# Optimization experiments

Hardware: AMD Instinct MI355X
Metric: run time of the kernel (lower is better)

The kernel has to match this reference:

```python
import jax, jax.numpy as jnp
import numpy as np

N, E, G = 10000, 160000, 64
NODE_DIM, HID = 128, 256


def _edge_conv(x, src, dst, w1, b1, w2, b2):
    # gather endpoints: x_i = target features, x_j = source features (PyG source_to_target)
    x_i = x[dst]                              # [E, C]
    x_j = x[src]                              # [E, C]
    m = jnp.concatenate([x_i, x_j - x_i], axis=-1)  # [E, 2C]
    m = jax.nn.relu(m @ w1 + b1) @ w2 + b2          # [E, H]
    out = jax.ops.segment_max(m, dst, num_segments=N)  # scatter-max per target node
    return out  # nodes with no in-edges get -inf; subsequent relu maps them to 0 (matches PyG fill 0 + relu)


def setup_inputs() -> dict:
    key = jax.random.key(0)
    ks = jax.random.split(key, 20)
    x = jax.random.normal(ks[0], (N, NODE_DIM), dtype=jnp.float32)
    edge_index = jax.random.randint(ks[1], (2, E), 0, N)
    batch = jnp.sort(jax.random.randint(ks[2], (N,), 0, G))
    s = 0.05
    inp = {"x": x, "edge_index": edge_index, "batch": batch}
    dims = [(2 * NODE_DIM, HID), (2 * HID, HID), (2 * HID, HID)]
    for li, (din, dout) in enumerate(dims):
        inp[f"c{li}_w1"] = jax.random.normal(ks[3 + 4 * li], (din, dout), jnp.float32) * s
        inp[f"c{li}_b1"] = jnp.zeros((dout,), jnp.float32)
        inp[f"c{li}_w2"] = jax.random.normal(ks[4 + 4 * li], (dout, dout), jnp.float32) * s
        inp[f"c{li}_b2"] = jnp.zeros((dout,), jnp.float32)
    inp["cl_w1"] = jax.random.normal(ks[15], (2 * HID, HID), jnp.float32) * s
    inp["cl_b1"] = jnp.zeros((HID,), jnp.float32)
    inp["cl_w2"] = jax.random.normal(ks[16], (HID, 64), jnp.float32) * s
    inp["cl_b2"] = jnp.zeros((64,), jnp.float32)
    inp["cl_w3"] = jax.random.normal(ks[17], (64, 1), jnp.float32) * s
    inp["cl_b3"] = jnp.zeros((1,), jnp.float32)
    return inp


def reference(x, edge_index, batch,
              c0_w1, c0_b1, c0_w2, c0_b2,
              c1_w1, c1_b1, c1_w2, c1_b2,
              c2_w1, c2_b1, c2_w2, c2_b2,
              cl_w1, cl_b1, cl_w2, cl_b2, cl_w3, cl_b3):
    src, dst = edge_index[0], edge_index[1]
    for (w1, b1, w2, b2) in [(c0_w1, c0_b1, c0_w2, c0_b2),
                             (c1_w1, c1_b1, c1_w2, c1_b2),
                             (c2_w1, c2_b1, c2_w2, c2_b2)]:
        x = jax.nn.relu(_edge_conv(x, src, dst, w1, b1, w2, b2))
    # global mean / max pool per graph
    sums = jax.ops.segment_sum(x, batch, num_segments=G)
    counts = jax.ops.segment_sum(jnp.ones((x.shape[0], 1), x.dtype), batch, num_segments=G)
    x_mean = sums / jnp.maximum(counts, 1.0)
    x_max = jax.ops.segment_max(x, batch, num_segments=G)
    x_max = jnp.where(counts > 0, x_max, 0.0)
    h = jnp.concatenate([x_mean, x_max], axis=1)  # [G, 2H]
    h = jax.nn.relu(h @ cl_w1 + cl_b1)            # dropout is eval-mode identity
    h = jax.nn.relu(h @ cl_w2 + cl_b2)
    out = (h @ cl_w3 + cl_b3).squeeze(-1)         # [G]
    return out
```

## Files before the change

### kernel.cpp

```cpp
#include <hip/hip_runtime.h>


#define NN 10000
#define NE 160000
#define NG 64
#define NP 10048
#define EB 64

typedef __attribute__((ext_vector_type(8))) _Float16 f16x8;
typedef __attribute__((ext_vector_type(4))) _Float16 f16x4;
typedef __attribute__((ext_vector_type(4))) float f32x4;

__global__ void hist_kernel(const int* __restrict__ dstI, int* __restrict__ hist) {
    int i = blockIdx.x * blockDim.x + threadIdx.x;
    if (i < NE) atomicAdd(&hist[dstI[i]], 1);
}

__global__ void scan_kernel(const int* __restrict__ hist, int* __restrict__ cursor) {
    __shared__ int sums[256];
    const int t = threadIdx.x;
    const int per = (NN + 255) / 256;
    const int lo = t * per, hi = (lo + per < NN) ? lo + per : NN;
    int s = 0;
    for (int i = lo; i < hi; ++i) s += hist[i];
    sums[t] = s;
    __syncthreads();
    for (int ofs = 1; ofs < 256; ofs <<= 1) {
        int add = (t >= ofs) ? sums[t - ofs] : 0;
        __syncthreads();
        sums[t] += add;
        __syncthreads();
    }
    int run = sums[t] - s;
    for (int i = lo; i < hi; ++i) {
        int h = hist[i];
        cursor[i] = run;
        run += h;
    }
}

__global__ void scatter_kernel(const int* __restrict__ srcI, const int* __restrict__ dstI,
                               int* __restrict__ cursor,
                               int* __restrict__ se2, int* __restrict__ de2) {
    int i = blockIdx.x * blockDim.x + threadIdx.x;
    if (i < NE) {
        int d = dstI[i];
        int p = atomicAdd(&cursor[d], 1);
        se2[p] = srcI[i];
        de2[p] = d;
    }
}

__global__ void prep_weights(const float* __restrict__ w1, const float* __restrict__ w2, int C,
                             _Float16* __restrict__ WcT, _Float16* __restrict__ w2T) {
    int total1 = 512 * C;
    int total = total1 + 256 * 256;
    for (int i = blockIdx.x * blockDim.x + threadIdx.x; i < total; i += gridDim.x * blockDim.x) {
        if (i < total1) {
            int n = i / C, k = i - n * C;
            float v = (n < 256) ? (w1[k * 256 + n] - w1[(C + k) * 256 + n])
                                : w1[(C + k) * 256 + (n - 256)];
            WcT[n * C + k] = (_Float16)v;
        } else {
            int j = i - total1;
            int n = j >> 8, k = j & 255;
            w2T[n * 256 + k] = (_Float16)w2[k * 256 + n];
        }
    }
}

template <int C>
__global__ __launch_bounds__(256) void node_gemm(
    const float* __restrict__ xf, const _Float16* __restrict__ WT,
    const float* __restrict__ b1, float* __restrict__ Af, _Float16* __restrict__ Bh) {
    const int wave = threadIdx.x >> 6, lane = threadIdx.x & 63;
    const int lrow = lane & 15, lk = (lane >> 4) * 8;
    const int r0 = blockIdx.x * 64;
    const int c0 = blockIdx.y * 256 + wave * 64;

    f32x4 acc[4][4] = {};
#pragma unroll
    for (int kk = 0; kk < C; kk += 32) {
        f16x8 ah[4];
#pragma unroll
        for (int m = 0; m < 4; ++m) {
            int rc = r0 + m * 16 + lrow;
            if (rc > NN - 1) rc = NN - 1;
            const float* xp = xf + (size_t)rc * C + kk + lk;
            const float4 v0 = *(const float4*)(xp);
            const float4 v1 = *(const float4*)(xp + 4);
            f16x8 a;
            a[0] = (_Float16)v0.x; a[1] = (_Float16)v0.y;
            a[2] = (_Float16)v0.z; a[3] = (_Float16)v0.w;
            a[4] = (_Float16)v1.x; a[5] = (_Float16)v1.y;
            a[6] = (_Float16)v1.z; a[7] = (_Float16)v1.w;
            ah[m] = a;
        }
#pragma unroll
        for (int t = 0; t < 4; ++t) {
            f16x8 bh = *(const f16x8*)(WT + (size_t)(c0 + t * 16 + lrow) * C + kk + lk);
#pragma unroll
            for (int m = 0; m < 4; ++m)
                acc[m][t] = __builtin_amdgcn_mfma_f32_16x16x32_f16(ah[m], bh, acc[m][t], 0, 0, 0);
        }
    }
    if (blockIdx.y == 0) {
#pragma unroll
        for (int t = 0; t < 4; ++t) {
            const int col = c0 + t * 16 + lrow;
            const float bias = b1[col];
#pragma unroll
            for (int m = 0; m < 4; ++m)
#pragma unroll
                for (int j = 0; j < 4; ++j) {
                    const int row = r0 + m * 16 + (lane >> 4) * 4 + j;
                    Af[(size_t)row * 256 + col] = acc[m][t][j] + bias;
                }
        }
    } else {
#pragma unroll
        for (int t = 0; t < 4; ++t) {
            const int col = c0 - 256 + t * 16 + lrow;
#pragma unroll
            for (int m = 0; m < 4; ++m)
#pragma unroll
                for (int j = 0; j < 4; ++j) {
                    const int row = r0 + m * 16 + (lane >> 4) * 4 + j;
                    Bh[(size_t)row * 256 + col] = (_Float16)acc[m][t][j];
                }
        }
    }
}

__global__ __launch_bounds__(512, 4) void edge_gemm(
    const float* __restrict__ Af, const _Float16* __restrict__ Bh,
    const int* __restrict__ se2, const int* __restrict__ de2,
    const _Float16* __restrict__ w2T,
    const float* __restrict__ b2, float* __restrict__ y) {
    __shared__ _Float16 hh[EB * 256];
    const int tid = threadIdx.x;
    const int wave = tid >> 6, lane = tid & 63;

    const int orig = blockIdx.x;
    const int xcd = orig & 7, pos = orig >> 3;
    const int qq = 2500 >> 3, rr = 2500 & 7;
    const int bid = (xcd < rr ? xcd * (qq + 1) : rr * (qq + 1) + (xcd - rr) * qq) + pos;
    const int e0 = bid * EB;

    const int lrow = lane & 15, lk = (lane >> 4) * 8;
    const _Float16* wbase = w2T + (size_t)(wave * 32 + lrow) * 256 + lk;

    f16x8 w0[8], w1[8];

    {
        int se[8], de[8];
#pragma unroll
        for (int i = 0; i < 8; ++i) {
            se[i] = se2[e0 + wave * 8 + i];
            de[i] = de2[e0 + wave * 8 + i];
        }
        float4 av[8];
        f16x4 bv[8];
#pragma unroll
        for (int i = 0; i < 8; ++i) {
            bv[i] = *(const f16x4*)(Bh + (size_t)se[i] * 256 + lane * 4);
            av[i] = *(const float4*)(Af + (size_t)de[i] * 256 + lane * 4);
        }
#pragma unroll
        for (int q = 0; q < 4; ++q) {
            w0[q]     = *(const f16x8*)(wbase + q * 32);
            w0[4 + q] = *(const f16x8*)(wbase + 16 * 256 + q * 32);
        }
#pragma unroll
        for (int i = 0; i < 8; ++i) {
            const int el = wave * 8 + i;
            const int row = ((el >> 2) & 3) * 16 + (el >> 4) * 4 + (el & 3);
            f16x4 vh;
            vh[0] = (_Float16)fmaxf(av[i].x + (float)bv[i][0], 0.f);
            vh[1] = (_Float16)fmaxf(av[i].y + (float)bv[i][1], 0.f);
            vh[2] = (_Float16)fmaxf(av[i].z + (float)bv[i][2], 0.f);
            vh[3] = (_Float16)fmaxf(av[i].w + (float)bv[i][3], 0.f);
            const int idx = (row * 256 + lane * 4) ^ ((row & 7) << 3);
            *(f16x4*)(&hh[idx]) = vh;
        }
    }
    __syncthreads();

#pragma unroll
    for (int q = 0; q < 4; ++q) {
        w1[q]     = *(const f16x8*)(wbase + 128 + q * 32);
        w1[4 + q] = *(const f16x8*)(wbase + 16 * 256 + 128 + q * 32);
    }

    f32x4 acc[4][2] = {};
#pragma unroll
    for (int q = 0; q < 4; ++q) {
        const int kk = q * 32;
        f16x8 ah[4];
#pragma unroll
        for (int m = 0; m < 4; ++m) {
            const int row = m * 16 + lrow;
            const int idx = (row * 256 + kk + lk) ^ ((row & 7) << 3);
            ah[m] = *(const f16x8*)(&hh[idx]);
        }
#pragma unroll
        for (int m = 0; m < 4; ++m) {
            acc[m][0] = __builtin_amdgcn_mfma_f32_16x16x32_f16(ah[m], w0[q],     acc[m][0], 0, 0, 0);
            acc[m][1] = __builtin_amdgcn_mfma_f32_16x16x32_f16(ah[m], w0[4 + q], acc[m][1], 0, 0, 0);
        }
    }
#pragma unroll
    for (int q = 0; q < 4; ++q) {
        const int kk = 128 + q * 32;
        f16x8 ah[4];
#pragma unroll
        for (int m = 0; m < 4; ++m) {
            const int row = m * 16 + lrow;
            const int idx = (row * 256 + kk + lk) ^ ((row & 7) << 3);
            ah[m] = *(const f16x8*)(&hh[idx]);
        }
#pragma unroll
        for (int m = 0; m < 4; ++m) {
            acc[m][0] = __builtin_amdgcn_mfma_f32_16x16x32_f16(ah[m], w1[q],     acc[m][0], 0, 0, 0);
            acc[m][1] = __builtin_amdgcn_mfma_f32_16x16x32_f16(ah[m], w1[4 + q], acc[m][1], 0, 0, 0);
        }
    }

    const int g = lane >> 4;
    int d[16];
#pragma unroll
    for (int k = 0; k < 16; ++k) d[k] = de2[e0 + g * 16 + k];
#pragma unroll
    for (int t = 0; t < 2; ++t) {
        const int col = wave * 32 + t * 16 + lrow;
        const float bias = b2[col];
        float run = acc[0][t][0];
        int dp = d[0];
#pragma unroll
        for (int k = 1; k < 16; ++k) {
            const float v = acc[k >> 2][t][k & 3];
            if (d[k] == dp) {
                run = fmaxf(run, v);
            } else {
                const float o = run + bias;
                if (o > 0.f) atomicMax((int*)(y + (size_t)dp * 256 + col), __float_as_int(o));
                run = v;
                dp = d[k];
            }
        }
        const float o = run + bias;
        if (o > 0.f) atomicMax((int*)(y + (size_t)dp * 256 + col), __float_as_int(o));
    }
}

__global__ void pool_kernel(const float* __restrict__ y, const int* __restrict__ batch,
                            float* __restrict__ pooled) {
    const int g = blockIdx.x;
    __shared__ int slo, shi;
    if (threadIdx.x == 0) {
        int lo = 0, hi = NN;
        while (lo < hi) { int m = (lo + hi) >> 1; if (batch[m] < g) lo = m + 1; else hi = m; }
        slo = lo;
        int lo2 = lo, hi2 = NN;
        while (lo2 < hi2) { int m = (lo2 + hi2) >> 1; if (batch[m] < g + 1) lo2 = m + 1; else hi2 = m; }
        shi = lo2;
    }
    __syncthreads();
    const int lo = slo, hi = shi, c = threadIdx.x;
    float s0 = 0.f, s1 = 0.f, s2 = 0.f, s3 = 0.f;
    float m0 = 0.f, m1 = 0.f, m2 = 0.f, m3 = 0.f;
    int n = lo;
    for (; n + 4 <= hi; n += 4) {
        float v0 = y[(size_t)(n + 0) * 256 + c];
        float v1 = y[(size_t)(n + 1) * 256 + c];
        float v2 = y[(size_t)(n + 2) * 256 + c];
        float v3 = y[(size_t)(n + 3) * 256 + c];
        s0 += v0; s1 += v1; s2 += v2; s3 += v3;
        m0 = fmaxf(m0, v0); m1 = fmaxf(m1, v1); m2 = fmaxf(m2, v2); m3 = fmaxf(m3, v3);
    }
    for (; n < hi; ++n) {
        float v = y[(size_t)n * 256 + c];
        s0 += v; m0 = fmaxf(m0, v);
    }
    const float s = (s0 + s1) + (s2 + s3);
    const float mx = fmaxf(fmaxf(m0, m1), fmaxf(m2, m3));
    const int cnt = hi - lo;
    pooled[g * 512 + c] = cnt ? s / (float)cnt : 0.f;
    pooled[g * 512 + 256 + c] = cnt ? mx : 0.f;
}

__global__ void classifier(const float* __restrict__ pooled,
                           const float* __restrict__ w1, const float* __restrict__ b1,
                           const float* __restrict__ w2, const float* __restrict__ b2,
                           const float* __restrict__ w3, const float* __restrict__ b3,
                           float* __restrict__ out) {
    const int g = blockIdx.x;
    __shared__ float ph[512];
    __shared__ float o1[256];
    __shared__ float o2[64];
    const int t = threadIdx.x;
    ph[t] = pooled[g * 512 + t];
    ph[t + 256] = pooled[g * 512 + 256 + t];
    __syncthreads();
    float s = 0.f;
    for (int k = 0; k < 512; ++k) s += ph[k] * w1[k * 256 + t];
    o1[t] = fmaxf(s + b1[t], 0.f);
    __syncthreads();
    if (t < 64) {
        float s2 = 0.f;
        for (int k = 0; k < 256; ++k) s2 += o1[k] * w2[k * 64 + t];
        o2[t] = fmaxf(s2 + b2[t], 0.f);
    }
    __syncthreads();
    if (t < 64) {
        float v = o2[t] * w3[t];
        for (int off = 32; off; off >>= 1) v += __shfl_down(v, off);
        if (t == 0) out[g] = v + b3[0];
    }
}

extern "C" void kernel_launch(void* const* d_in, const int* in_sizes, int n_in,
                              void* d_out, int out_size, void* d_ws, size_t ws_size,
                              hipStream_t stream) {
    (void)in_sizes; (void)n_in; (void)out_size; (void)ws_size;
    const float* x0 = (const float*)d_in[0];
    const int* eidx = (const int*)d_in[1];
    const int* batch = (const int*)d_in[2];
    const int* srcI = eidx;
    const int* dstI = eidx + NE;

    char* ws = (char*)d_ws;
    size_t off = 0;
    auto alloc = [&](size_t bytes) -> void* {
        void* p = ws + off;
        off += (bytes + 255) & ~(size_t)255;
        return p;
    };
    float* Af = (float*)alloc((size_t)NP * 256 * 4);
    _Float16* Bh = (_Float16*)alloc((size_t)NP * 256 * 2);
    float* y  = (float*)alloc((size_t)NP * 256 * 4);
    _Float16* WcT = (_Float16*)alloc(512 * 256 * 2);
    _Float16* w2T = (_Float16*)alloc(256 * 256 * 2);
    float* pooled = (float*)alloc(64 * 512 * 4);
    int* hist = (int*)alloc(NN * 4);
    int* se2 = (int*)alloc(NE * 4);
    int* de2 = (int*)alloc(NE * 4);

    const float* lw[3][4] = {
        {(const float*)d_in[3],  (const float*)d_in[4],  (const float*)d_in[5],  (const float*)d_in[6]},
        {(const float*)d_in[7],  (const float*)d_in[8],  (const float*)d_in[9],  (const float*)d_in[10]},
        {(const float*)d_in[11], (const float*)d_in[12], (const float*)d_in[13], (const float*)d_in[14]},
    };

    hipMemsetAsync(hist, 0, NN * 4, stream);
    hist_kernel<<<dim3((NE + 255) / 256), dim3(256), 0, stream>>>(dstI, hist);
    scan_kernel<<<dim3(1), dim3(256), 0, stream>>>(hist, hist);
    scatter_kernel<<<dim3((NE + 255) / 256), dim3(256), 0, stream>>>(srcI, dstI, hist, se2, de2);

    for (int l = 0; l < 3; ++l) {
        const int C = (l == 0) ? 128 : 256;
        prep_weights<<<dim3(256), dim3(256), 0, stream>>>(lw[l][0], lw[l][2], C, WcT, w2T);
        if (C == 128)
            node_gemm<128><<<dim3(NP / 64, 2), dim3(256), 0, stream>>>(x0, WcT, lw[l][1], Af, Bh);
        else
            node_gemm<256><<<dim3(NP / 64, 2), dim3(256), 0, stream>>>(y, WcT, lw[l][1], Af, Bh);
        hipMemsetAsync(y, 0, (size_t)NP * 256 * 4, stream);
        edge_gemm<<<dim3(NE / EB), dim3(512), 0, stream>>>(Af, Bh, se2, de2, w2T, lw[l][3], y);
    }

    pool_kernel<<<dim3(NG), dim3(256), 0, stream>>>(y, batch, pooled);
    classifier<<<dim3(NG), dim3(256), 0, stream>>>(pooled,
        (const float*)d_in[15], (const float*)d_in[16],
        (const float*)d_in[17], (const float*)d_in[18],
        (const float*)d_in[19], (const float*)d_in[20], (float*)d_out);
}
```

Baseline: 365.3 us.

## Persistent double-buffered edge GEMM, fp16 node projections, wider pool and node_gemm grid

The edge kernel becomes persistent: 500 blocks each process 5 edge tiles. The gather for the next tile is issued before the current MFMA pass, and a double-buffered LDS array holds the staged tiles. The second-layer weights are loaded into registers once per block. The node-side projection A is now stored as fp16, which halves gather traffic and drops fp32 loads, at some precision cost. node_gemm is split into 4 column blocks with a smaller accumulator for more occupancy, and pool_kernel uses 4 row groups per graph with a shared-memory reduction.

```diff
diff --git a/kernel.cpp b/kernel.cpp
--- a/kernel.cpp
+++ b/kernel.cpp
@@ -6,6 +6,8 @@
 #define NG 64
 #define NP 10048
 #define EB 64
+#define TPB 5
+#define NBLK 500
 
 typedef __attribute__((ext_vector_type(8))) _Float16 f16x8;
 typedef __attribute__((ext_vector_type(4))) _Float16 f16x4;
@@ -70,15 +72,15 @@
 }
 
 template <int C>
-__global__ __launch_bounds__(256) void node_gemm(
+__global__ __launch_bounds__(256, 4) void node_gemm(
     const float* __restrict__ xf, const _Float16* __restrict__ WT,
-    const float* __restrict__ b1, float* __restrict__ Af, _Float16* __restrict__ Bh) {
+    const float* __restrict__ b1, _Float16* __restrict__ Afh, _Float16* __restrict__ Bh) {
     const int wave = threadIdx.x >> 6, lane = threadIdx.x & 63;
     const int lrow = lane & 15, lk = (lane >> 4) * 8;
     const int r0 = blockIdx.x * 64;
-    const int c0 = blockIdx.y * 256 + wave * 64;
-
-    f32x4 acc[4][4] = {};
+    const int c0 = blockIdx.y * 128 + wave * 32;
+
+    f32x4 acc[4][2] = {};
 #pragma unroll
     for (int kk = 0; kk < C; kk += 32) {
         f16x8 ah[4];
@@ -97,16 +99,16 @@
             ah[m] = a;
         }
 #pragma unroll
-        for (int t = 0; t < 4; ++t) {
+        for (int t = 0; t < 2; ++t) {
             f16x8 bh = *(const f16x8*)(WT + (size_t)(c0 + t * 16 + lrow) * C + kk + lk);
 #pragma unroll
             for (int m = 0; m < 4; ++m)
                 acc[m][t] = __builtin_amdgcn_mfma_f32_16x16x32_f16(ah[m], bh, acc[m][t], 0, 0, 0);
         }
     }
-    if (blockIdx.y == 0) {
-#pragma unroll
-        for (int t = 0; t < 4; ++t) {
+    if (blockIdx.y < 2) {
+#pragma unroll
+        for (int t = 0; t < 2; ++t) {
             const int col = c0 + t * 16 + lrow;
             const float bias = b1[col];
 #pragma unroll
@@ -114,12 +116,12 @@
 #pragma unroll
                 for (int j = 0; j < 4; ++j) {
                     const int row = r0 + m * 16 + (lane >> 4) * 4 + j;
-                    Af[(size_t)row * 256 + col] = acc[m][t][j] + bias;
+                    Afh[(size_t)row * 256 + col] = (_Float16)(acc[m][t][j] + bias);
                 }
         }
     } else {
 #pragma unroll
-        for (int t = 0; t < 4; ++t) {
+        for (int t = 0; t < 2; ++t) {
             const int col = c0 - 256 + t * 16 + lrow;
 #pragma unroll
             for (int m = 0; m < 4; ++m)
@@ -132,124 +134,123 @@
     }
 }
 
-__global__ __launch_bounds__(512, 4) void edge_gemm(
-    const float* __restrict__ Af, const _Float16* __restrict__ Bh,
+__global__ __launch_bounds__(512, 3) void edge_gemm(
+    const _Float16* __restrict__ Afh, const _Float16* __restrict__ Bh,
     const int* __restrict__ se2, const int* __restrict__ de2,
     const _Float16* __restrict__ w2T,
     const float* __restrict__ b2, float* __restrict__ y) {
-    __shared__ _Float16 hh[EB * 256];
+    __shared__ _Float16 hh[2 * EB * 256];
     const int tid = threadIdx.x;
     const int wave = tid >> 6, lane = tid & 63;
+    const int lrow = lane & 15, lk = (lane >> 4) * 8;
 
     const int orig = blockIdx.x;
     const int xcd = orig & 7, pos = orig >> 3;
-    const int qq = 2500 >> 3, rr = 2500 & 7;
+    const int qq = NBLK >> 3, rr = NBLK & 7;
     const int bid = (xcd < rr ? xcd * (qq + 1) : rr * (qq + 1) + (xcd - rr) * qq) + pos;
-    const int e0 = bid * EB;
-
-    const int lrow = lane & 15, lk = (lane >> 4) * 8;
+    const int t0 = bid * TPB;
+
+    f16x8 w[16];
     const _Float16* wbase = w2T + (size_t)(wave * 32 + lrow) * 256 + lk;
-
-    f16x8 w0[8], w1[8];
-
-    {
-        int se[8], de[8];
+#pragma unroll
+    for (int q = 0; q < 8; ++q) {
+        w[q]     = *(const f16x8*)(wbase + q * 32);
+        w[8 + q] = *(const f16x8*)(wbase + 16 * 256 + q * 32);
+    }
+
+    f16x4 av[8], bv[8];
+    int se[8], de[8];
+
+    auto stage_issue = [&](int tile) {
 #pragma unroll
         for (int i = 0; i < 8; ++i) {
-            se[i] = se2[e0 + wave * 8 + i];
-            de[i] = de2[e0 + wave * 8 + i];
-        }
-        float4 av[8];
-        f16x4 bv[8];
+            const int e = tile * EB + wave * 8 + i;
+            se[i] = se2[e];
+            de[i] = de2[e];
+        }
 #pragma unroll
         for (int i = 0; i < 8; ++i) {
             bv[i] = *(const f16x4*)(Bh + (size_t)se[i] * 256 + lane * 4);
-            av[i] = *(const float4*)(Af + (size_t)de[i] * 256 + lane * 4);
-        }
-#pragma unroll
-        for (int q = 0; q < 4; ++q) {
-            w0[q]     = *(const f16x8*)(wbase + q * 32);
-            w0[4 + q] = *(const f16x8*)(wbase + 16 * 256 + q * 32);
-        }
+            av[i] = *(const f16x4*)(Afh + (size_t)de[i] * 256 + lane * 4);
+        }
+    };
+    auto stage_write = [&](int buf) {
 #pragma unroll
         for (int i = 0; i < 8; ++i) {
             const int el = wave * 8 + i;
             const int row = ((el >> 2) & 3) * 16 + (el >> 4) * 4 + (el & 3);
-            f16x4 vh;
-            vh[0] = (_Float16)fmaxf(av[i].x + (float)bv[i][0], 0.f);
-            vh[1] = (_Float16)fmaxf(av[i].y + (float)bv[i][1], 0.f);
-            vh[2] = (_Float16)fmaxf(av[i].z + (float)bv[i][2], 0.f);
-            vh[3] = (_Float16)fmaxf(av[i].w + (float)bv[i][3], 0.f);
-            const int idx = (row * 256 + lane * 4) ^ ((row & 7) << 3);
-            *(f16x4*)(&hh[idx]) = vh;
-        }
-    }
-    __syncthreads();
-
-#pragma unroll
-    for (int q = 0; q < 4; ++q) {
-        w1[q]     = *(const f16x8*)(wbase + 128 + q * 32);
-        w1[4 + q] = *(const f16x8*)(wbase + 16 * 256 + 128 + q * 32);
-    }
-
-    f32x4 acc[4][2] = {};
-#pragma unroll
-    for (int q = 0; q < 4; ++q) {
-        const int kk = q * 32;
-        f16x8 ah[4];
-#pragma unroll
-        for (int m = 0; m < 4; ++m) {
-            const int row = m * 16 + lrow;
-            const int idx = (row * 256 + kk + lk) ^ ((row & 7) << 3);
-            ah[m] = *(const f16x8*)(&hh[idx]);
-        }
-#pragma unroll
-        for (int m = 0; m < 4; ++m) {
-            acc[m][0] = __builtin_amdgcn_mfma_f32_16x16x32_f16(ah[m], w0[q],     acc[m][0], 0, 0, 0);
-            acc[m][1] = __builtin_amdgcn_mfma_f32_16x16x32_f16(ah[m], w0[4 + q], acc[m][1], 0, 0, 0);
-        }
-    }
-#pragma unroll
-    for (int q = 0; q < 4; ++q) {
-        const int kk = 128 + q * 32;
-        f16x8 ah[4];
-#pragma unroll
-        for (int m = 0; m < 4; ++m) {
-            const int row = m * 16 + lrow;
-            const int idx = (row * 256 + kk + lk) ^ ((row & 7) << 3);
-            ah[m] = *(const f16x8*)(&hh[idx]);
-        }
-#pragma unroll
-        for (int m = 0; m < 4; ++m) {
-            acc[m][0] = __builtin_amdgcn_mfma_f32_16x16x32_f16(ah[m], w1[q],     acc[m][0], 0, 0, 0);
-            acc[m][1] = __builtin_amdgcn_mfma_f32_16x16x32_f16(ah[m], w1[4 + q], acc[m][1], 0, 0, 0);
-        }
-    }
-
-    const int g = lane >> 4;
-    int d[16];
-#pragma unroll
-    for (int k = 0; k < 16; ++k) d[k] = de2[e0 + g * 16 + k];
-#pragma unroll
-    for (int t = 0; t < 2; ++t) {
-        const int col = wave * 32 + t * 16 + lrow;
-        const float bias = b2[col];
-        float run = acc[0][t][0];
-        int dp = d[0];
-#pragma unroll
-        for (int k = 1; k < 16; ++k) {
-            const float v = acc[k >> 2][t][k & 3];
-            if (d[k] == dp) {
-                run = fmaxf(run, v);
-            } else {
+            f16x4 h = av[i] + bv[i];
+#pragma unroll
+            for (int k = 0; k < 4; ++k) h[k] = h[k] > (_Float16)0.f ? h[k] : (_Float16)0.f;
+            *(f16x4*)(&hh[buf * (EB * 256) + ((row * 256 + lane * 4) ^ ((row & 7) << 3))]) = h;
+        }
+    };
+
+    stage_issue(t0);
+    stage_write(0);
+    __syncthreads();
+
+#pragma unroll
+    for (int q = 0; q < 16; ++q) {
+        f32x4 tmp = __builtin_bit_cast(f32x4, w[q]);
+        asm volatile("" : "+v"(tmp));
+        w[q] = __builtin_bit_cast(f16x8, tmp);
+    }
+
+    for (int tt = 0; tt < TPB; ++tt) {
+        const int tile = t0 + tt;
+        const int hbase = (tt & 1) * (EB * 256);
+
+        if (tt + 1 < TPB) stage_issue(tile + 1);
+
+        f32x4 acc[4][2] = {};
+#pragma unroll
+        for (int q = 0; q < 8; ++q) {
+            f16x8 ah[4];
+#pragma unroll
+            for (int m = 0; m < 4; ++m) {
+                const int row = m * 16 + lrow;
+                const int idx = (row * 256 + q * 32 + lk) ^ ((row & 7) << 3);
+                ah[m] = *(const f16x8*)(&hh[hbase + idx]);
+            }
+#pragma unroll
+            for (int m = 0; m < 4; ++m) {
+                acc[m][0] = __builtin_amdgcn_mfma_f32_16x16x32_f16(ah[m], w[q],     acc[m][0], 0, 0, 0);
+                acc[m][1] = __builtin_amdgcn_mfma_f32_16x16x32_f16(ah[m], w[8 + q], acc[m][1], 0, 0, 0);
+            }
+        }
+
+        {
+            const int g = lane >> 4;
+            const int e0 = tile * EB;
+            int d[16];
+#pragma unroll
+            for (int k = 0; k < 16; ++k) d[k] = de2[e0 + g * 16 + k];
+#pragma unroll
+            for (int t = 0; t < 2; ++t) {
+                const int col = wave * 32 + t * 16 + lrow;
+                const float bias = b2[col];
+                float run = acc[0][t][0];
+                int dp = d[0];
+#pragma unroll
+                for (int k = 1; k < 16; ++k) {
+                    const float v = acc[k >> 2][t][k & 3];
+                    if (d[k] == dp) {
+                        run = fmaxf(run, v);
+                    } else {
+                        const float o = run + bias;
+                        if (o > 0.f) atomicMax((int*)(y + (size_t)dp * 256 + col), __float_as_int(o));
+                        run = v;
+                        dp = d[k];
+                    }
+                }
                 const float o = run + bias;
                 if (o > 0.f) atomicMax((int*)(y + (size_t)dp * 256 + col), __float_as_int(o));
-                run = v;
-                dp = d[k];
             }
         }
-        const float o = run + bias;
-        if (o > 0.f) atomicMax((int*)(y + (size_t)dp * 256 + col), __float_as_int(o));
+
+        if (tt + 1 < TPB) stage_write((tt + 1) & 1);
+        __syncthreads();
     }
 }
 
@@ -257,7 +258,10 @@
                             float* __restrict__ pooled) {
     const int g = blockIdx.x;
     __shared__ int slo, shi;
-    if (threadIdx.x == 0) {
+    __shared__ float ssum[4][256];
+    __shared__ float smax[4][256];
+    const int c = threadIdx.x, ry = threadIdx.y;
+    if (c == 0 && ry == 0) {
         int lo = 0, hi = NN;
         while (lo < hi) { int m = (lo + hi) >> 1; if (batch[m] < g) lo = m + 1; else hi = m; }
         slo = lo;
@@ -266,27 +270,23 @@
         shi = lo2;
     }
     __syncthreads();
-    const int lo = slo, hi = shi, c = threadIdx.x;
-    float s0 = 0.f, s1 = 0.f, s2 = 0.f, s3 = 0.f;
-    float m0 = 0.f, m1 = 0.f, m2 = 0.f, m3 = 0.f;
-    int n = lo;
-    for (; n + 4 <= hi; n += 4) {
-        float v0 = y[(size_t)(n + 0) * 256 + c];
-        float v1 = y[(size_t)(n + 1) * 256 + c];
-        float v2 = y[(size_t)(n + 2) * 256 + c];
-        float v3 = y[(size_t)(n + 3) * 256 + c];
-        s0 += v0; s1 += v1; s2 += v2; s3 += v3;
-        m0 = fmaxf(m0, v0); m1 = fmaxf(m1, v1); m2 = fmaxf(m2, v2); m3 = fmaxf(m3, v3);
-    }
-    for (; n < hi; ++n) {
-        float v = y[(size_t)n * 256 + c];
-        s0 += v; m0 = fmaxf(m0, v);
-    }
-    const float s = (s0 + s1) + (s2 + s3);
-    const float mx = fmaxf(fmaxf(m0, m1), fmaxf(m2, m3));
-    const int cnt = hi - lo;
-    pooled[g * 512 + c] = cnt ? s / (float)cnt : 0.f;
-    pooled[g * 512 + 256 + c] = cnt ? mx : 0.f;
+    const int lo = slo, hi = shi;
+    float s = 0.f, mx = 0.f;
+    for (int n = lo + ry; n < hi; n += 4) {
+        const float v = y[(size_t)n * 256 + c];
+        s += v;
+        mx = fmaxf(mx, v);
+    }
+    ssum[ry][c] = s;
+    smax[ry][c] = mx;
+    __syncthreads();
+    if (ry == 0) {
+        const float st = (ssum[0][c] + ssum[1][c]) + (ssum[2][c] + ssum[3][c]);
+        const float mt = fmaxf(fmaxf(smax[0][c], smax[1][c]), fmaxf(smax[2][c], smax[3][c]));
+        const int cnt = hi - lo;
+        pooled[g * 512 + c] = cnt ? st / (float)cnt : 0.f;
+        pooled[g * 512 + 256 + c] = cnt ? mt : 0.f;
+    }
 }
 
 __global__ void classifier(const float* __restrict__ pooled,
@@ -336,8 +336,8 @@
         off += (bytes + 255) & ~(size_t)255;
         return p;
     };
-    float* Af = (float*)alloc((size_t)NP * 256 * 4);
-    _Float16* Bh = (_Float16*)alloc((size_t)NP * 256 * 2);
+    _Float16* Afh = (_Float16*)alloc((size_t)NP * 256 * 2);
+    _Float16* Bh  = (_Float16*)alloc((size_t)NP * 256 * 2);
     float* y  = (float*)alloc((size_t)NP * 256 * 4);
     _Float16* WcT = (_Float16*)alloc(512 * 256 * 2);
     _Float16* w2T = (_Float16*)alloc(256 * 256 * 2);
@@ -361,14 +361,14 @@
         const int C = (l == 0) ? 128 : 256;
         prep_weights<<<dim3(256), dim3(256), 0, stream>>>(lw[l][0], lw[l][2], C, WcT, w2T);
         if (C == 128)
-            node_gemm<128><<<dim3(NP / 64, 2), dim3(256), 0, stream>>>(x0, WcT, lw[l][1], Af, Bh);
+            node_gemm<128><<<dim3(NP / 64, 4), dim3(256), 0, stream>>>(x0, WcT, lw[l][1], Afh, Bh);
         else
-            node_gemm<256><<<dim3(NP / 64, 2), dim3(256), 0, stream>>>(y, WcT, lw[l][1], Af, Bh);
+            node_gemm<256><<<dim3(NP / 64, 4), dim3(256), 0, stream>>>(y, WcT, lw[l][1], Afh, Bh);
         hipMemsetAsync(y, 0, (size_t)NP * 256 * 4, stream);
-        edge_gemm<<<dim3(NE / EB), dim3(512), 0, stream>>>(Af, Bh, se2, de2, w2T, lw[l][3], y);
-    }
-
-    pool_kernel<<<dim3(NG), dim3(256), 0, stream>>>(y, batch, pooled);
+        edge_gemm<<<dim3(NBLK), dim3(512), 0, stream>>>(Afh, Bh, se2, de2, w2T, lw[l][3], y);
+    }
+
+    pool_kernel<<<dim3(NG), dim3(256, 4), 0, stream>>>(y, batch, pooled);
     classifier<<<dim3(NG), dim3(256), 0, stream>>>(pooled,
         (const float*)d_in[15], (const float*)d_in[16],
         (const float*)d_in[17], (const float*)d_in[18],
```

After: 535.3 us. 1.47x slower.
